# Performance work log

Hardware: AMD Instinct MI355X
Metric: run time of the kernel (lower is better)

The kernel has to match this reference:

```python
import jax, jax.numpy as jnp
import numpy as np

N_NODES = 100000


def gcn_conv(x, edge_index, W, b):
    # PyG GCNConv: add self-loops, symmetric norm, then scatter-aggregate.
    n = x.shape[0]
    x = x @ W  # [N, out]
    src = jnp.concatenate([edge_index[0], jnp.arange(n)])  # self-loops
    dst = jnp.concatenate([edge_index[1], jnp.arange(n)])
    ones = jnp.ones(src.shape[0], dtype=x.dtype)
    deg = jax.ops.segment_sum(ones, dst, num_segments=n)  # in-degree incl. self-loops
    dis = jnp.where(deg > 0, jax.lax.rsqrt(deg), 0.0)
    norm = dis[src] * dis[dst]  # [E+N]
    msg = x[src] * norm[:, None]  # gather + scale
    out = jax.ops.segment_sum(msg, dst, num_segments=n)
    return out + b


def setup_inputs() -> dict:
    key = jax.random.key(0)
    ks = jax.random.split(key, 8)
    in_dim, h1, h2, out_dim, E = 128, 128, 64, 10, 1600000
    glorot = lambda k, fi, fo: jax.random.normal(k, (fi, fo), jnp.float32) * np.sqrt(2.0 / (fi + fo))
    return {
        "x": jax.random.normal(ks[0], (N_NODES, in_dim), jnp.float32),
        "edge_index": jax.random.randint(ks[1], (2, E), 0, N_NODES, jnp.int64),
        "W1": glorot(ks[2], in_dim, h1),
        "b1": jnp.zeros((h1,), jnp.float32),
        "W2": glorot(ks[3], h1, h2),
        "b2": jnp.zeros((h2,), jnp.float32),
        "Wf": glorot(ks[4], h2, out_dim),
        "bf": jnp.zeros((out_dim,), jnp.float32),
    }


def reference(x, edge_index, W1, b1, W2, b2, Wf, bf):
    h = jax.nn.relu(gcn_conv(x, edge_index, W1, b1))
    h = jax.nn.relu(gcn_conv(h, edge_index, W2, b2))
    logits = h @ Wf + bf
    return jax.nn.softmax(logits, axis=1)
```

## Files before the change

### kernel.cpp

```cpp
#include <hip/hip_runtime.h>
#include <math.h>

#define NN 100000
#define D_IN 128
#define D_H1 128
#define D_H2 64
#define D_O 10
#define NB 256
#define BDIV 391
#define ECH 2048
#define COLCAP 8192

static const size_t OFF_G1     = 0;
static const size_t OFF_H1     = 51200000;
static const size_t OFF_PART   = 76800000;
static const size_t OFF_COL    = 102400000;
static const size_t OFF_DIS    = 108800000;
static const size_t OFF_ROWPTR = 109300000;
static const size_t OFF_HIST   = 109800000;
static const size_t OFF_TOT    = 110700000;
static const size_t OFF_BASE   = 110710000;

typedef __attribute__((ext_vector_type(8))) short short8;
typedef __attribute__((ext_vector_type(4))) float floatx4;

__device__ inline unsigned int pack_bf2(float a, float b) {
  unsigned int ua = __float_as_uint(a);
  ua += 0x7fffu + ((ua >> 16) & 1u);
  unsigned int ub = __float_as_uint(b);
  ub += 0x7fffu + ((ub >> 16) & 1u);
  return (ua >> 16) | (ub & 0xffff0000u);
}
__device__ inline unsigned short bf16u(float a) {
  unsigned int ua = __float_as_uint(a);
  ua += 0x7fffu + ((ua >> 16) & 1u);
  return (unsigned short)(ua >> 16);
}
__device__ inline float bflo(unsigned int u) { return __uint_as_float(u << 16); }
__device__ inline float bfhi(unsigned int u) { return __uint_as_float(u & 0xffff0000u); }
__device__ inline short8 as_short8(uint4 u) {
  union { uint4 u4; short8 s8; } c; c.u4 = u; return c.s8;
}
__device__ inline void acc_u4(float* acc, uint4 u) {
  acc[0] += bflo(u.x); acc[1] += bfhi(u.x);
  acc[2] += bflo(u.y); acc[3] += bfhi(u.y);
  acc[4] += bflo(u.z); acc[5] += bfhi(u.z);
  acc[6] += bflo(u.w); acc[7] += bfhi(u.w);
}

__global__ __launch_bounds__(256) void histo_kernel(
    const int* __restrict__ dst, int* __restrict__ H, int E, int nchunk) {
  __shared__ int hist[NB];
  const int tid = threadIdx.x;
  hist[tid] = 0;
  __syncthreads();
  const int e0 = blockIdx.x * ECH;
#pragma unroll
  for (int i = 0; i < ECH / 256; ++i) {
    int e = e0 + i * 256 + tid;
    if (e < E) atomicAdd(&hist[dst[e] / BDIV], 1);
  }
  __syncthreads();
  H[tid * nchunk + blockIdx.x] = hist[tid];
}

__global__ __launch_bounds__(256) void bucket_scan_kernel(
    int* __restrict__ H, int* __restrict__ total, int nchunk) {
  __shared__ int sm[256];
  const int tid = threadIdx.x;
  int* row = H + (size_t)blockIdx.x * nchunk;
  int carry = 0;
  for (int t0 = 0; t0 < nchunk; t0 += 256) {
    int idx = t0 + tid;
    int v = (idx < nchunk) ? row[idx] : 0;
    sm[tid] = v;
    __syncthreads();
#pragma unroll
    for (int off = 1; off < 256; off <<= 1) {
      int t2 = (tid >= off) ? sm[tid - off] : 0;
      __syncthreads();
      sm[tid] += t2;
      __syncthreads();
    }
    int incl = sm[tid];
    int ttot = sm[255];
    __syncthreads();
    if (idx < nchunk) row[idx] = carry + incl - v;
    carry += ttot;
  }
  if (tid == 0) total[blockIdx.x] = carry;
}

__global__ __launch_bounds__(256) void base_scan_kernel(
    const int* __restrict__ total, int* __restrict__ base) {
  __shared__ int sm[256];
  const int tid = threadIdx.x;
  int v = total[tid];
  sm[tid] = v;
  __syncthreads();
#pragma unroll
  for (int off = 1; off < 256; off <<= 1) {
    int t2 = (tid >= off) ? sm[tid - off] : 0;
    __syncthreads();
    sm[tid] += t2;
    __syncthreads();
  }
  base[tid] = sm[tid] - v;
  if (tid == 255) base[256] = sm[255];
}

__global__ __launch_bounds__(256) void scatter_kernel(
    const int* __restrict__ src, const int* __restrict__ dst,
    const int* __restrict__ H, const int* __restrict__ base,
    int2* __restrict__ part, int E, int nchunk) {
  __shared__ int offs_s[NB];
  __shared__ int base_s[NB];
  __shared__ int cnt[NB];
  const int tid = threadIdx.x;
  offs_s[tid] = H[tid * nchunk + blockIdx.x];
  base_s[tid] = base[tid];
  cnt[tid] = 0;
  __syncthreads();
  const int e0 = blockIdx.x * ECH;
#pragma unroll
  for (int i = 0; i < ECH / 256; ++i) {
    int e = e0 + i * 256 + tid;
    if (e < E) {
      int d = dst[e];
      int s = src[e];
      int b = d / BDIV;
      int r = atomicAdd(&cnt[b], 1);
      part[(size_t)base_s[b] + offs_s[b] + r] = make_int2(d, s);
    }
  }
}

__global__ __launch_bounds__(256) void bucket_csr_kernel(
    const int2* __restrict__ part, const int* __restrict__ base,
    int* __restrict__ row_ptr, float* __restrict__ dis,
    int* __restrict__ col, int n, int E) {
  __shared__ int sm[256];
  __shared__ int ldeg[BDIV + 1];
  __shared__ int lofs[BDIV + 1];
  __shared__ int col_s[COLCAP];
  const int tid = threadIdx.x;
  const int b = blockIdx.x;
  const int lo = b * BDIV;
  const int nn = min(n - lo, BDIV);
  const int ebase = base[b];
  const int ecnt = base[b + 1] - ebase;

  for (int t = tid; t <= BDIV; t += 256) ldeg[t] = 0;
  __syncthreads();
  for (int i0 = 0; i0 < ecnt; i0 += 256) {
    int idx = i0 + tid;
    if (idx < ecnt) atomicAdd(&ldeg[part[ebase + idx].x - lo], 1);
  }
  __syncthreads();
  int carry = 0;
  for (int t0 = 0; t0 < BDIV + 1; t0 += 256) {
    int idx = t0 + tid;
    int v = (idx <= BDIV) ? ldeg[idx] : 0;
    sm[tid] = v;
    __syncthreads();
#pragma unroll
    for (int off = 1; off < 256; off <<= 1) {
      int t2 = (tid >= off) ? sm[tid - off] : 0;
      __syncthreads();
      sm[tid] += t2;
      __syncthreads();
    }
    int incl = sm[tid];
    int ttot = sm[255];
    __syncthreads();
    if (idx <= BDIV) lofs[idx] = carry + incl - v;
    carry += ttot;
  }
  __syncthreads();
  for (int t = tid; t < nn; t += 256) {
    row_ptr[lo + t] = ebase + lofs[t];
    dis[lo + t] = rsqrtf((float)ldeg[t] + 1.0f);
  }
  if (b == NB - 1 && tid == 0) row_ptr[n] = E;
  __syncthreads();
  for (int i0 = 0; i0 < ecnt; i0 += 256) {
    int idx = i0 + tid;
    if (idx < ecnt) {
      int2 p = part[ebase + idx];
      int r = atomicAdd(&lofs[p.x - lo], 1);
      if (r < COLCAP) col_s[r] = p.y;
    }
  }
  __syncthreads();
  const int m = min(ecnt, COLCAP);
  for (int idx = tid; idx < m; idx += 256) col[ebase + idx] = col_s[idx];
}

template <int NOUT, bool IN_BF>
__global__ __launch_bounds__(256) void gemm_mfma_kernel(
    const void* __restrict__ A_, const float* __restrict__ W,
    const float* __restrict__ dis, unsigned short* __restrict__ out, int nrows) {
  constexpr int K = 128;
  constexpr int NT = NOUT / 16;
  constexpr int LDW = K + 8;
  __shared__ unsigned short wt[NOUT * LDW];
  __shared__ unsigned short buf[4 * 16 * LDW];
  const int tid = threadIdx.x;

  {
    constexpr int NGRP = 256 / NOUT;
    constexpr int KG = K / NGRP;
    int n = tid % NOUT;
    int k0 = (tid / NOUT) * KG;
#pragma unroll
    for (int kb = 0; kb < KG / 8; ++kb) {
      int k = k0 + kb * 8;
      unsigned int u0 = pack_bf2(W[(size_t)(k + 0) * NOUT + n], W[(size_t)(k + 1) * NOUT + n]);
      unsigned int u1 = pack_bf2(W[(size_t)(k + 2) * NOUT + n], W[(size_t)(k + 3) * NOUT + n]);
      unsigned int u2 = pack_bf2(W[(size_t)(k + 4) * NOUT + n], W[(size_t)(k + 5) * NOUT + n]);
      unsigned int u3 = pack_bf2(W[(size_t)(k + 6) * NOUT + n], W[(size_t)(k + 7) * NOUT + n]);
      *(uint4*)(wt + n * LDW + k) = make_uint4(u0, u1, u2, u3);
    }
  }

  const int wave = tid >> 6;
  const int lane = tid & 63;
  const int quad = lane >> 4;
  const int cg = lane & 15;
  const int row0w = blockIdx.x * 64 + wave * 16;

  short8 afr[4];
  {
    int row = row0w + cg;
    if (row > nrows - 1) row = nrows - 1;
    if (IN_BF) {
      const unsigned short* Au = (const unsigned short*)A_;
#pragma unroll
      for (int kb = 0; kb < 4; ++kb)
        afr[kb] = as_short8(*(const uint4*)(Au + (size_t)row * K + kb * 32 + quad * 8));
    } else {
      const float* Af = (const float*)A_;
#pragma unroll
      for (int kb = 0; kb < 4; ++kb) {
        const float* p = Af + (size_t)row * K + kb * 32 + quad * 8;
        float4 v0 = *(const float4*)(p);
        float4 v1 = *(const float4*)(p + 4);
        uint4 u;
        u.x = pack_bf2(v0.x, v0.y); u.y = pack_bf2(v0.z, v0.w);
        u.z = pack_bf2(v1.x, v1.y); u.w = pack_bf2(v1.z, v1.w);
        afr[kb] = as_short8(u);
      }
    }
  }
  __syncthreads();

  floatx4 acc[NT];
#pragma unroll
  for (int t = 0; t < NT; ++t) acc[t] = (floatx4){0.f, 0.f, 0.f, 0.f};
#pragma unroll
  for (int t = 0; t < NT; ++t) {
    const unsigned short* wrow = wt + (t * 16 + cg) * LDW;
#pragma unroll
    for (int kb = 0; kb < 4; ++kb) {
      short8 bfr = *(const short8*)(wrow + kb * 32 + quad * 8);
      acc[t] = __builtin_amdgcn_mfma_f32_16x16x32_bf16(afr[kb], bfr, acc[t], 0, 0, 0);
    }
  }

  float4 dv4 = *(const float4*)(dis + row0w + quad * 4);
  float dvs[4] = {dv4.x, dv4.y, dv4.z, dv4.w};
  unsigned short* mybuf = buf + wave * 16 * LDW;
#pragma unroll
  for (int t = 0; t < NT; ++t)
#pragma unroll
    for (int r = 0; r < 4; ++r)
      mybuf[(quad * 4 + r) * LDW + t * 16 + cg] = bf16u(acc[t][r] * dvs[r]);
  __syncthreads();

  constexpr int CHUNKS = NOUT / 8;
  constexpr int RPI = 64 / CHUNKS;
  int cid = lane % CHUNKS;
  int rs = lane / CHUNKS;
#pragma unroll
  for (int i = 0; i < 16 / RPI; ++i) {
    int r = rs + i * RPI;
    int grow = row0w + r;
    if (grow < nrows) {
      uint4 u = *(const uint4*)(mybuf + r * LDW + cid * 8);
      *(uint4*)(out + (size_t)grow * NOUT + cid * 8) = u;
    }
  }
}

template <int F, int LOG_LPN>
__global__ __launch_bounds__(256) void gather_bf_kernel(
    const unsigned short* __restrict__ g, const int* __restrict__ col,
    const int* __restrict__ row_ptr, const float* __restrict__ dis,
    const float* __restrict__ b, unsigned short* __restrict__ h, int n) {
  constexpr int LPN = 1 << LOG_LPN;
  int gid = blockIdx.x * 256 + threadIdx.x;
  int v = gid >> LOG_LPN;
  if (v >= n) return;
  int c = (gid & (LPN - 1)) * 8;
  int start = row_ptr[v];
  int end = row_ptr[v + 1];
  float acc[8];
  acc_u4(acc, *(const uint4*)(g + (size_t)v * F + c));
  {
#pragma unroll
    for (int q = 0; q < 8; ++q) acc[q] = 0.f;
    acc_u4(acc, *(const uint4*)(g + (size_t)v * F + c));
  }
  int e = start;
  for (; e + 4 <= end; e += 4) {
    int s0 = col[e + 0], s1 = col[e + 1], s2 = col[e + 2], s3 = col[e + 3];
    uint4 u0 = *(const uint4*)(g + (size_t)s0 * F + c);
    uint4 u1 = *(const uint4*)(g + (size_t)s1 * F + c);
    uint4 u2 = *(const uint4*)(g + (size_t)s2 * F + c);
    uint4 u3 = *(const uint4*)(g + (size_t)s3 * F + c);
    acc_u4(acc, u0); acc_u4(acc, u1); acc_u4(acc, u2); acc_u4(acc, u3);
  }
  for (; e < end; ++e) {
    uint4 u = *(const uint4*)(g + (size_t)col[e] * F + c);
    acc_u4(acc, u);
  }
  float dv = dis[v];
  float4 bv0 = *(const float4*)(b + c);
  float4 bv1 = *(const float4*)(b + c + 4);
  float r0 = fmaxf(dv * acc[0] + bv0.x, 0.f);
  float r1 = fmaxf(dv * acc[1] + bv0.y, 0.f);
  float r2 = fmaxf(dv * acc[2] + bv0.z, 0.f);
  float r3 = fmaxf(dv * acc[3] + bv0.w, 0.f);
  float r4 = fmaxf(dv * acc[4] + bv1.x, 0.f);
  float r5 = fmaxf(dv * acc[5] + bv1.y, 0.f);
  float r6 = fmaxf(dv * acc[6] + bv1.z, 0.f);
  float r7 = fmaxf(dv * acc[7] + bv1.w, 0.f);
  uint4 o;
  o.x = pack_bf2(r0, r1);
  o.y = pack_bf2(r2, r3);
  o.z = pack_bf2(r4, r5);
  o.w = pack_bf2(r6, r7);
  *(uint4*)(h + (size_t)v * F + c) = o;
}

__global__ __launch_bounds__(256) void gather2_final_kernel(
    const unsigned short* __restrict__ g, const int* __restrict__ col,
    const int* __restrict__ row_ptr, const float* __restrict__ dis,
    const float* __restrict__ b2, const float* __restrict__ Wf,
    const float* __restrict__ bf, float* __restrict__ out, int n) {
  __shared__ float hs[32][68];
  __shared__ float wfs[D_H2 * D_O];
  __shared__ float bfs[D_O];
  __shared__ float ls[32][12];
  const int tid = threadIdx.x;
  for (int i = tid; i < D_H2 * D_O; i += 256) wfs[i] = Wf[i];
  if (tid < D_O) bfs[tid] = bf[tid];

  const int gid = blockIdx.x * 256 + tid;
  const int v = gid >> 3;
  const int nl = tid >> 3;
  const int c = (tid & 7) * 8;
  if (v < n) {
    int start = row_ptr[v];
    int end = row_ptr[v + 1];
    float acc[8];
#pragma unroll
    for (int q = 0; q < 8; ++q) acc[q] = 0.f;
    acc_u4(acc, *(const uint4*)(g + (size_t)v * D_H2 + c));
    int e = start;
    for (; e + 4 <= end; e += 4) {
      int s0 = col[e + 0], s1 = col[e + 1], s2 = col[e + 2], s3 = col[e + 3];
      uint4 u0 = *(const uint4*)(g + (size_t)s0 * D_H2 + c);
      uint4 u1 = *(const uint4*)(g + (size_t)s1 * D_H2 + c);
      uint4 u2 = *(const uint4*)(g + (size_t)s2 * D_H2 + c);
      uint4 u3 = *(const uint4*)(g + (size_t)s3 * D_H2 + c);
      acc_u4(acc, u0); acc_u4(acc, u1); acc_u4(acc, u2); acc_u4(acc, u3);
    }
    for (; e < end; ++e) {
      uint4 u = *(const uint4*)(g + (size_t)col[e] * D_H2 + c);
      acc_u4(acc, u);
    }
    float dv = dis[v];
    float4 bv0 = *(const float4*)(b2 + c);
    float4 bv1 = *(const float4*)(b2 + c + 4);
    hs[nl][c + 0] = fmaxf(dv * acc[0] + bv0.x, 0.f);
    hs[nl][c + 1] = fmaxf(dv * acc[1] + bv0.y, 0.f);
    hs[nl][c + 2] = fmaxf(dv * acc[2] + bv0.z, 0.f);
    hs[nl][c + 3] = fmaxf(dv * acc[3] + bv0.w, 0.f);
    hs[nl][c + 4] = fmaxf(dv * acc[4] + bv1.x, 0.f);
    hs[nl][c + 5] = fmaxf(dv * acc[5] + bv1.y, 0.f);
    hs[nl][c + 6] = fmaxf(dv * acc[6] + bv1.z, 0.f);
    hs[nl][c + 7] = fmaxf(dv * acc[7] + bv1.w, 0.f);
  }
  __syncthreads();
  for (int idx = tid; idx < 32 * D_O; idx += 256) {
    int n2 = idx / D_O;
    int j = idx % D_O;
    int v2 = blockIdx.x * 32 + n2;
    if (v2 < n) {
      float acc = bfs[j];
#pragma unroll 8
      for (int k = 0; k < D_H2; ++k) acc += hs[n2][k] * wfs[k * D_O + j];
      ls[n2][j] = acc;
    }
  }
  __syncthreads();
  if (tid < 32) {
    int v2 = blockIdx.x * 32 + tid;
    if (v2 < n) {
      float m = ls[tid][0];
#pragma unroll
      for (int j = 1; j < D_O; ++j) m = fmaxf(m, ls[tid][j]);
      float s = 0.f;
      float ex[D_O];
#pragma unroll
      for (int j = 0; j < D_O; ++j) { ex[j] = expf(ls[tid][j] - m); s += ex[j]; }
      float inv = 1.0f / s;
#pragma unroll
      for (int j = 0; j < D_O; ++j) ls[tid][j] = ex[j] * inv;
    }
  }
  __syncthreads();
  for (int idx = tid; idx < 32 * D_O; idx += 256) {
    int gidx = blockIdx.x * 32 * D_O + idx;
    if (gidx < n * D_O) out[gidx] = ls[idx / D_O][idx % D_O];
  }
}

extern "C" void kernel_launch(void* const* d_in, const int* in_sizes, int n_in,
                              void* d_out, int out_size, void* d_ws, size_t ws_size,
                              hipStream_t stream) {
  const float* x  = (const float*)d_in[0];
  const int*   ei = (const int*)d_in[1];
  const float* W1 = (const float*)d_in[2];
  const float* b1 = (const float*)d_in[3];
  const float* W2 = (const float*)d_in[4];
  const float* b2 = (const float*)d_in[5];
  const float* Wf = (const float*)d_in[6];
  const float* bf = (const float*)d_in[7];
  float* out = (float*)d_out;

  const int E = in_sizes[1] / 2;
  const int* src = ei;
  const int* dst = ei + E;

  char* ws = (char*)d_ws;
  unsigned short* g1 = (unsigned short*)(ws + OFF_G1);
  unsigned short* h1 = (unsigned short*)(ws + OFF_H1);
  int2*  part    = (int2*)(ws + OFF_PART);
  int*   col     = (int*)(ws + OFF_COL);
  float* dis     = (float*)(ws + OFF_DIS);
  int*   row_ptr = (int*)(ws + OFF_ROWPTR);
  int*   H       = (int*)(ws + OFF_HIST);
  int*   total   = (int*)(ws + OFF_TOT);
  int*   base    = (int*)(ws + OFF_BASE);
  unsigned short* g2 = (unsigned short*)(ws + OFF_G1);

  const int nchunk = (E + ECH - 1) / ECH;

  histo_kernel<<<nchunk, 256, 0, stream>>>(dst, H, E, nchunk);
  bucket_scan_kernel<<<NB, 256, 0, stream>>>(H, total, nchunk);
  base_scan_kernel<<<1, 256, 0, stream>>>(total, base);
  scatter_kernel<<<nchunk, 256, 0, stream>>>(src, dst, H, base, part, E, nchunk);
  bucket_csr_kernel<<<NB, 256, 0, stream>>>(part, base, row_ptr, dis, col, NN, E);

  gemm_mfma_kernel<D_H1, false>
      <<<(NN + 63) / 64, 256, 0, stream>>>(x, W1, dis, g1, NN);
  gather_bf_kernel<D_H1, 4>
      <<<((size_t)NN * 16 + 255) / 256, 256, 0, stream>>>(g1, col, row_ptr, dis, b1, h1, NN);

  gemm_mfma_kernel<D_H2, true>
      <<<(NN + 63) / 64, 256, 0, stream>>>(h1, W2, dis, g2, NN);

  gather2_final_kernel<<<(NN + 31) / 32, 256, 0, stream>>>(
      g2, col, row_ptr, dis, b2, Wf, bf, out, NN);
}
```

Baseline: 263.1 us.

## Partition layer-1 gather by feature slice per XCD with persistent work queues

New measurement: 501.5 us. 90.6% more time.

```diff
diff --git a/kernel.cpp b/kernel.cpp
--- a/kernel.cpp
+++ b/kernel.cpp
@@ -10,6 +10,7 @@
 #define BDIV 391
 #define ECH 2048
 #define COLCAP 8192
+#define NCHN ((NN + 255) / 256)
 
 static const size_t OFF_G1     = 0;
 static const size_t OFF_H1     = 51200000;
@@ -20,6 +21,7 @@
 static const size_t OFF_HIST   = 109800000;
 static const size_t OFF_TOT    = 110700000;
 static const size_t OFF_BASE   = 110710000;
+static const size_t OFF_WQ     = 110715000;
 
 typedef __attribute__((ext_vector_type(8))) short short8;
 typedef __attribute__((ext_vector_type(4))) float floatx4;
@@ -46,6 +48,12 @@
   acc[2] += bflo(u.y); acc[3] += bfhi(u.y);
   acc[4] += bflo(u.z); acc[5] += bfhi(u.z);
   acc[6] += bflo(u.w); acc[7] += bfhi(u.w);
+}
+
+__device__ inline int get_xcc() {
+  int x;
+  asm volatile("s_getreg_b32 %0, hwreg(HW_REG_XCC_ID, 0, 4)" : "=s"(x));
+  return x & 7;
 }
 
 __global__ __launch_bounds__(256) void histo_kernel(
@@ -292,55 +300,75 @@
   }
 }
 
-template <int F, int LOG_LPN>
-__global__ __launch_bounds__(256) void gather_bf_kernel(
+__global__ __launch_bounds__(256) void gather1_xcd_kernel(
     const unsigned short* __restrict__ g, const int* __restrict__ col,
     const int* __restrict__ row_ptr, const float* __restrict__ dis,
-    const float* __restrict__ b, unsigned short* __restrict__ h, int n) {
-  constexpr int LPN = 1 << LOG_LPN;
-  int gid = blockIdx.x * 256 + threadIdx.x;
-  int v = gid >> LOG_LPN;
-  if (v >= n) return;
-  int c = (gid & (LPN - 1)) * 8;
-  int start = row_ptr[v];
-  int end = row_ptr[v + 1];
-  float acc[8];
-  acc_u4(acc, *(const uint4*)(g + (size_t)v * F + c));
-  {
-#pragma unroll
-    for (int q = 0; q < 8; ++q) acc[q] = 0.f;
-    acc_u4(acc, *(const uint4*)(g + (size_t)v * F + c));
-  }
-  int e = start;
-  for (; e + 4 <= end; e += 4) {
-    int s0 = col[e + 0], s1 = col[e + 1], s2 = col[e + 2], s3 = col[e + 3];
-    uint4 u0 = *(const uint4*)(g + (size_t)s0 * F + c);
-    uint4 u1 = *(const uint4*)(g + (size_t)s1 * F + c);
-    uint4 u2 = *(const uint4*)(g + (size_t)s2 * F + c);
-    uint4 u3 = *(const uint4*)(g + (size_t)s3 * F + c);
-    acc_u4(acc, u0); acc_u4(acc, u1); acc_u4(acc, u2); acc_u4(acc, u3);
-  }
-  for (; e < end; ++e) {
-    uint4 u = *(const uint4*)(g + (size_t)col[e] * F + c);
-    acc_u4(acc, u);
-  }
-  float dv = dis[v];
-  float4 bv0 = *(const float4*)(b + c);
-  float4 bv1 = *(const float4*)(b + c + 4);
-  float r0 = fmaxf(dv * acc[0] + bv0.x, 0.f);
-  float r1 = fmaxf(dv * acc[1] + bv0.y, 0.f);
-  float r2 = fmaxf(dv * acc[2] + bv0.z, 0.f);
-  float r3 = fmaxf(dv * acc[3] + bv0.w, 0.f);
-  float r4 = fmaxf(dv * acc[4] + bv1.x, 0.f);
-  float r5 = fmaxf(dv * acc[5] + bv1.y, 0.f);
-  float r6 = fmaxf(dv * acc[6] + bv1.z, 0.f);
-  float r7 = fmaxf(dv * acc[7] + bv1.w, 0.f);
-  uint4 o;
-  o.x = pack_bf2(r0, r1);
-  o.y = pack_bf2(r2, r3);
-  o.z = pack_bf2(r4, r5);
-  o.w = pack_bf2(r6, r7);
-  *(uint4*)(h + (size_t)v * F + c) = o;
+    const float* __restrict__ b, unsigned short* __restrict__ h,
+    int* __restrict__ wq, int n) {
+  __shared__ int chunk_s;
+  const int tid = threadIdx.x;
+  const int x = get_xcc();
+#pragma unroll 1
+  for (int pass = 0; pass < 8; ++pass) {
+    const int f = (x + pass) & 7;
+    const int c0 = f * 16;
+#pragma unroll 1
+    while (true) {
+      __syncthreads();
+      if (tid == 0) chunk_s = atomicAdd(&wq[f], 1);
+      __syncthreads();
+      const int c = chunk_s;
+      if (c >= NCHN) break;
+      const int v = c * 256 + tid;
+      if (v < n) {
+        const int start = row_ptr[v];
+        const int end = row_ptr[v + 1];
+        float acc[16];
+#pragma unroll
+        for (int q = 0; q < 16; ++q) acc[q] = 0.f;
+        {
+          const unsigned short* gv = g + (size_t)v * D_H1 + c0;
+          acc_u4(acc, *(const uint4*)(gv));
+          acc_u4(acc + 8, *(const uint4*)(gv + 8));
+        }
+        int e = start;
+        for (; e + 2 <= end; e += 2) {
+          int s0 = col[e], s1 = col[e + 1];
+          const unsigned short* p0 = g + (size_t)s0 * D_H1 + c0;
+          const unsigned short* p1 = g + (size_t)s1 * D_H1 + c0;
+          uint4 u00 = *(const uint4*)(p0);
+          uint4 u01 = *(const uint4*)(p0 + 8);
+          uint4 u10 = *(const uint4*)(p1);
+          uint4 u11 = *(const uint4*)(p1 + 8);
+          acc_u4(acc, u00); acc_u4(acc + 8, u01);
+          acc_u4(acc, u10); acc_u4(acc + 8, u11);
+        }
+        for (; e < end; ++e) {
+          const unsigned short* p0 = g + (size_t)col[e] * D_H1 + c0;
+          acc_u4(acc, *(const uint4*)(p0));
+          acc_u4(acc + 8, *(const uint4*)(p0 + 8));
+        }
+        const float dv = dis[v];
+        float r[16];
+#pragma unroll
+        for (int q = 0; q < 4; ++q) {
+          float4 bv = *(const float4*)(b + c0 + q * 4);
+          r[q * 4 + 0] = fmaxf(dv * acc[q * 4 + 0] + bv.x, 0.f);
+          r[q * 4 + 1] = fmaxf(dv * acc[q * 4 + 1] + bv.y, 0.f);
+          r[q * 4 + 2] = fmaxf(dv * acc[q * 4 + 2] + bv.z, 0.f);
+          r[q * 4 + 3] = fmaxf(dv * acc[q * 4 + 3] + bv.w, 0.f);
+        }
+        uint4 o0, o1;
+        o0.x = pack_bf2(r[0], r[1]);  o0.y = pack_bf2(r[2], r[3]);
+        o0.z = pack_bf2(r[4], r[5]);  o0.w = pack_bf2(r[6], r[7]);
+        o1.x = pack_bf2(r[8], r[9]);  o1.y = pack_bf2(r[10], r[11]);
+        o1.z = pack_bf2(r[12], r[13]); o1.w = pack_bf2(r[14], r[15]);
+        unsigned short* hp = h + (size_t)v * D_H1 + c0;
+        *(uint4*)(hp) = o0;
+        *(uint4*)(hp + 8) = o1;
+      }
+    }
+  }
 }
 
 __global__ __launch_bounds__(256) void gather2_final_kernel(
@@ -454,6 +482,7 @@
   int*   H       = (int*)(ws + OFF_HIST);
   int*   total   = (int*)(ws + OFF_TOT);
   int*   base    = (int*)(ws + OFF_BASE);
+  int*   wq      = (int*)(ws + OFF_WQ);
   unsigned short* g2 = (unsigned short*)(ws + OFF_G1);
 
   const int nchunk = (E + ECH - 1) / ECH;
@@ -463,11 +492,11 @@
   base_scan_kernel<<<1, 256, 0, stream>>>(total, base);
   scatter_kernel<<<nchunk, 256, 0, stream>>>(src, dst, H, base, part, E, nchunk);
   bucket_csr_kernel<<<NB, 256, 0, stream>>>(part, base, row_ptr, dis, col, NN, E);
+  hipMemsetAsync(wq, 0, 8 * 4, stream);
 
   gemm_mfma_kernel<D_H1, false>
       <<<(NN + 63) / 64, 256, 0, stream>>>(x, W1, dis, g1, NN);
-  gather_bf_kernel<D_H1, 4>
-      <<<((size_t)NN * 16 + 255) / 256, 256, 0, stream>>>(g1, col, row_ptr, dis, b1, h1, NN);
+  gather1_xcd_kernel<<<1024, 256, 0, stream>>>(g1, col, row_ptr, dis, b1, h1, wq, NN);
 
   gemm_mfma_kernel<D_H2, true>
       <<<(NN + 63) / 64, 256, 0, stream>>>(h1, W2, dis, g2, NN);
```

## Fuse layer-1 gather aggregation with layer-2 MFMA GEMM in one kernel

Applied to the files above, without the earlier changes.

New measurement: 254.1 us. -3.4%, faster.

```diff
diff --git a/kernel.cpp b/kernel.cpp
--- a/kernel.cpp
+++ b/kernel.cpp
@@ -12,7 +12,6 @@
 #define COLCAP 8192
 
 static const size_t OFF_G1     = 0;
-static const size_t OFF_H1     = 51200000;
 static const size_t OFF_PART   = 76800000;
 static const size_t OFF_COL    = 102400000;
 static const size_t OFF_DIS    = 108800000;
@@ -20,6 +19,7 @@
 static const size_t OFF_HIST   = 109800000;
 static const size_t OFF_TOT    = 110700000;
 static const size_t OFF_BASE   = 110710000;
+static const size_t OFF_G2     = 25600000;
 
 typedef __attribute__((ext_vector_type(8))) short short8;
 typedef __attribute__((ext_vector_type(4))) float floatx4;
@@ -196,9 +196,9 @@
   for (int idx = tid; idx < m; idx += 256) col[ebase + idx] = col_s[idx];
 }
 
-template <int NOUT, bool IN_BF>
+template <int NOUT>
 __global__ __launch_bounds__(256) void gemm_mfma_kernel(
-    const void* __restrict__ A_, const float* __restrict__ W,
+    const float* __restrict__ A_, const float* __restrict__ W,
     const float* __restrict__ dis, unsigned short* __restrict__ out, int nrows) {
   constexpr int K = 128;
   constexpr int NT = NOUT / 16;
@@ -233,23 +233,15 @@
   {
     int row = row0w + cg;
     if (row > nrows - 1) row = nrows - 1;
-    if (IN_BF) {
-      const unsigned short* Au = (const unsigned short*)A_;
-#pragma unroll
-      for (int kb = 0; kb < 4; ++kb)
-        afr[kb] = as_short8(*(const uint4*)(Au + (size_t)row * K + kb * 32 + quad * 8));
-    } else {
-      const float* Af = (const float*)A_;
-#pragma unroll
-      for (int kb = 0; kb < 4; ++kb) {
-        const float* p = Af + (size_t)row * K + kb * 32 + quad * 8;
-        float4 v0 = *(const float4*)(p);
-        float4 v1 = *(const float4*)(p + 4);
-        uint4 u;
-        u.x = pack_bf2(v0.x, v0.y); u.y = pack_bf2(v0.z, v0.w);
-        u.z = pack_bf2(v1.x, v1.y); u.w = pack_bf2(v1.z, v1.w);
-        afr[kb] = as_short8(u);
-      }
+#pragma unroll
+    for (int kb = 0; kb < 4; ++kb) {
+      const float* p = A_ + (size_t)row * K + kb * 32 + quad * 8;
+      float4 v0 = *(const float4*)(p);
+      float4 v1 = *(const float4*)(p + 4);
+      uint4 u;
+      u.x = pack_bf2(v0.x, v0.y); u.y = pack_bf2(v0.z, v0.w);
+      u.z = pack_bf2(v1.x, v1.y); u.w = pack_bf2(v1.z, v1.w);
+      afr[kb] = as_short8(u);
     }
   }
   __syncthreads();
@@ -292,55 +284,104 @@
   }
 }
 
-template <int F, int LOG_LPN>
-__global__ __launch_bounds__(256) void gather_bf_kernel(
+__global__ __launch_bounds__(256) void gather1_gemm2_kernel(
     const unsigned short* __restrict__ g, const int* __restrict__ col,
     const int* __restrict__ row_ptr, const float* __restrict__ dis,
-    const float* __restrict__ b, unsigned short* __restrict__ h, int n) {
-  constexpr int LPN = 1 << LOG_LPN;
-  int gid = blockIdx.x * 256 + threadIdx.x;
-  int v = gid >> LOG_LPN;
-  if (v >= n) return;
-  int c = (gid & (LPN - 1)) * 8;
-  int start = row_ptr[v];
-  int end = row_ptr[v + 1];
-  float acc[8];
-  acc_u4(acc, *(const uint4*)(g + (size_t)v * F + c));
+    const float* __restrict__ b1, const float* __restrict__ W2,
+    unsigned short* __restrict__ g2, int n) {
+  constexpr int K = D_H1;
+  constexpr int LDW = K + 8;
+  constexpr int LDO = 80;
+  __shared__ unsigned short wt[D_H2 * LDW];
+  __shared__ unsigned short hl[16 * LDW];
+  __shared__ unsigned short obuf[16 * LDO];
+  const int tid = threadIdx.x;
+  const int row0 = blockIdx.x * 16;
+
   {
+    int nn = tid & 63;
+    int k0 = (tid >> 6) * 32;
+#pragma unroll
+    for (int kb = 0; kb < 4; ++kb) {
+      int k = k0 + kb * 8;
+      unsigned int u0 = pack_bf2(W2[(size_t)(k + 0) * D_H2 + nn], W2[(size_t)(k + 1) * D_H2 + nn]);
+      unsigned int u1 = pack_bf2(W2[(size_t)(k + 2) * D_H2 + nn], W2[(size_t)(k + 3) * D_H2 + nn]);
+      unsigned int u2 = pack_bf2(W2[(size_t)(k + 4) * D_H2 + nn], W2[(size_t)(k + 5) * D_H2 + nn]);
+      unsigned int u3 = pack_bf2(W2[(size_t)(k + 6) * D_H2 + nn], W2[(size_t)(k + 7) * D_H2 + nn]);
+      *(uint4*)(wt + nn * LDW + k) = make_uint4(u0, u1, u2, u3);
+    }
+  }
+
+  {
+    const int v = row0 + (tid >> 4);
+    const int c = (tid & 15) * 8;
+    const int start = row_ptr[v];
+    const int end = row_ptr[v + 1];
+    float acc[8];
 #pragma unroll
     for (int q = 0; q < 8; ++q) acc[q] = 0.f;
-    acc_u4(acc, *(const uint4*)(g + (size_t)v * F + c));
-  }
-  int e = start;
-  for (; e + 4 <= end; e += 4) {
-    int s0 = col[e + 0], s1 = col[e + 1], s2 = col[e + 2], s3 = col[e + 3];
-    uint4 u0 = *(const uint4*)(g + (size_t)s0 * F + c);
-    uint4 u1 = *(const uint4*)(g + (size_t)s1 * F + c);
-    uint4 u2 = *(const uint4*)(g + (size_t)s2 * F + c);
-    uint4 u3 = *(const uint4*)(g + (size_t)s3 * F + c);
-    acc_u4(acc, u0); acc_u4(acc, u1); acc_u4(acc, u2); acc_u4(acc, u3);
-  }
-  for (; e < end; ++e) {
-    uint4 u = *(const uint4*)(g + (size_t)col[e] * F + c);
-    acc_u4(acc, u);
-  }
-  float dv = dis[v];
-  float4 bv0 = *(const float4*)(b + c);
-  float4 bv1 = *(const float4*)(b + c + 4);
-  float r0 = fmaxf(dv * acc[0] + bv0.x, 0.f);
-  float r1 = fmaxf(dv * acc[1] + bv0.y, 0.f);
-  float r2 = fmaxf(dv * acc[2] + bv0.z, 0.f);
-  float r3 = fmaxf(dv * acc[3] + bv0.w, 0.f);
-  float r4 = fmaxf(dv * acc[4] + bv1.x, 0.f);
-  float r5 = fmaxf(dv * acc[5] + bv1.y, 0.f);
-  float r6 = fmaxf(dv * acc[6] + bv1.z, 0.f);
-  float r7 = fmaxf(dv * acc[7] + bv1.w, 0.f);
-  uint4 o;
-  o.x = pack_bf2(r0, r1);
-  o.y = pack_bf2(r2, r3);
-  o.z = pack_bf2(r4, r5);
-  o.w = pack_bf2(r6, r7);
-  *(uint4*)(h + (size_t)v * F + c) = o;
+    acc_u4(acc, *(const uint4*)(g + (size_t)v * K + c));
+    int e = start;
+    for (; e + 4 <= end; e += 4) {
+      int s0 = col[e + 0], s1 = col[e + 1], s2 = col[e + 2], s3 = col[e + 3];
+      uint4 u0 = *(const uint4*)(g + (size_t)s0 * K + c);
+      uint4 u1 = *(const uint4*)(g + (size_t)s1 * K + c);
+      uint4 u2 = *(const uint4*)(g + (size_t)s2 * K + c);
+      uint4 u3 = *(const uint4*)(g + (size_t)s3 * K + c);
+      acc_u4(acc, u0); acc_u4(acc, u1); acc_u4(acc, u2); acc_u4(acc, u3);
+    }
+    for (; e < end; ++e) {
+      uint4 u = *(const uint4*)(g + (size_t)col[e] * K + c);
+      acc_u4(acc, u);
+    }
+    float dv = dis[v];
+    float4 bv0 = *(const float4*)(b1 + c);
+    float4 bv1 = *(const float4*)(b1 + c + 4);
+    float r0 = fmaxf(dv * acc[0] + bv0.x, 0.f);
+    float r1 = fmaxf(dv * acc[1] + bv0.y, 0.f);
+    float r2 = fmaxf(dv * acc[2] + bv0.z, 0.f);
+    float r3 = fmaxf(dv * acc[3] + bv0.w, 0.f);
+    float r4 = fmaxf(dv * acc[4] + bv1.x, 0.f);
+    float r5 = fmaxf(dv * acc[5] + bv1.y, 0.f);
+    float r6 = fmaxf(dv * acc[6] + bv1.z, 0.f);
+    float r7 = fmaxf(dv * acc[7] + bv1.w, 0.f);
+    uint4 o;
+    o.x = pack_bf2(r0, r1);
+    o.y = pack_bf2(r2, r3);
+    o.z = pack_bf2(r4, r5);
+    o.w = pack_bf2(r6, r7);
+    *(uint4*)(hl + (tid >> 4) * LDW + c) = o;
+  }
+  __syncthreads();
+
+  {
+    const int wave = tid >> 6;
+    const int lane = tid & 63;
+    const int quad = lane >> 4;
+    const int cg = lane & 15;
+    floatx4 acc = (floatx4){0.f, 0.f, 0.f, 0.f};
+    const unsigned short* wrow = wt + (wave * 16 + cg) * LDW;
+    const unsigned short* arow = hl + cg * LDW;
+#pragma unroll
+    for (int kb = 0; kb < 4; ++kb) {
+      short8 afr = *(const short8*)(arow + kb * 32 + quad * 8);
+      short8 bfr = *(const short8*)(wrow + kb * 32 + quad * 8);
+      acc = __builtin_amdgcn_mfma_f32_16x16x32_bf16(afr, bfr, acc, 0, 0, 0);
+    }
+    float4 dv4 = *(const float4*)(dis + row0 + quad * 4);
+    float dvs[4] = {dv4.x, dv4.y, dv4.z, dv4.w};
+#pragma unroll
+    for (int r = 0; r < 4; ++r)
+      obuf[(quad * 4 + r) * LDO + wave * 16 + cg] = bf16u(acc[r] * dvs[r]);
+  }
+  __syncthreads();
+
+  if (tid < 128) {
+    int r = tid >> 3;
+    int cid = tid & 7;
+    uint4 u = *(const uint4*)(obuf + r * LDO + cid * 8);
+    *(uint4*)(g2 + (size_t)(row0 + r) * D_H2 + cid * 8) = u;
+  }
 }
 
 __global__ __launch_bounds__(256) void gather2_final_kernel(
@@ -446,7 +487,7 @@
 
   char* ws = (char*)d_ws;
   unsigned short* g1 = (unsigned short*)(ws + OFF_G1);
-  unsigned short* h1 = (unsigned short*)(ws + OFF_H1);
+  unsigned short* g2 = (unsigned short*)(ws + OFF_G2);
   int2*  part    = (int2*)(ws + OFF_PART);
   int*   col     = (int*)(ws + OFF_COL);
   float* dis     = (float*)(ws + OFF_DIS);
@@ -454,7 +495,6 @@
   int*   H       = (int*)(ws + OFF_HIST);
   int*   total   = (int*)(ws + OFF_TOT);
   int*   base    = (int*)(ws + OFF_BASE);
-  unsigned short* g2 = (unsigned short*)(ws + OFF_G1);
 
   const int nchunk = (E + ECH - 1) / ECH;
 
@@ -464,13 +504,11 @@
   scatter_kernel<<<nchunk, 256, 0, stream>>>(src, dst, H, base, part, E, nchunk);
   bucket_csr_kernel<<<NB, 256, 0, stream>>>(part, base, row_ptr, dis, col, NN, E);
 
-  gemm_mfma_kernel<D_H1, false>
+  gemm_mfma_kernel<D_H1>
       <<<(NN + 63) / 64, 256, 0, stream>>>(x, W1, dis, g1, NN);
-  gather_bf_kernel<D_H1, 4>
-      <<<((size_t)NN * 16 + 255) / 256, 256, 0, stream>>>(g1, col, row_ptr, dis, b1, h1, NN);
-
-  gemm_mfma_kernel<D_H2, true>
-      <<<(NN + 63) / 64, 256, 0, stream>>>(h1, W2, dis, g2, NN);
+
+  gather1_gemm2_kernel<<<NN / 16, 256, 0, stream>>>(
+      g1, col, row_ptr, dis, b1, W2, g2, NN);
 
   gather2_final_kernel<<<(NN + 31) / 32, 256, 0, stream>>>(
       g2, col, row_ptr, dis, b2, Wf, bf, out, NN);
```
